# Optimization experiments

Hardware: AMD Instinct MI355X
Metric: run time of the kernel (lower is better)

Reference implementation:

```python
import jax, jax.numpy as jnp
import numpy as np

DEPTH = 3
MAX_NB = 10

def setup_inputs() -> dict:
    key = jax.random.key(0)
    ks = jax.random.split(key, 10)
    B, N, NB, A, E, H = 64, 512, 600, 89, 5, 256
    input_atom = jax.random.normal(ks[0], (B, N, A), dtype=jnp.float32)
    input_bond = jax.random.normal(ks[1], (B, NB, E), dtype=jnp.float32)
    batch_idx = jnp.broadcast_to(jnp.arange(B, dtype=jnp.int32)[:, None, None], (B, N, MAX_NB))
    atom_nei = jax.random.randint(ks[2], (B, N, MAX_NB), 0, N, dtype=jnp.int32)
    bond_nei = jax.random.randint(ks[3], (B, N, MAX_NB), 0, NB, dtype=jnp.int32)
    atom_graph = jnp.stack([batch_idx, atom_nei], axis=-1)  # [B,N,MAX_NB,2]
    bond_graph = jnp.stack([batch_idx, bond_nei], axis=-1)
    num_nbs = jax.random.randint(ks[4], (B, N), 1, MAX_NB + 1, dtype=jnp.int32)
    s = 0.01
    W_atom = s * jax.random.normal(ks[5], (A, H), dtype=jnp.float32)
    W_U2 = s * jax.random.normal(ks[6], (H + E, H), dtype=jnp.float32)
    b_U2 = jnp.zeros((H,), dtype=jnp.float32)
    W_U1 = s * jax.random.normal(ks[7], (2 * H, H), dtype=jnp.float32)
    b_U1 = jnp.zeros((H,), dtype=jnp.float32)
    return {"input_atom": input_atom, "input_bond": input_bond,
            "atom_graph": atom_graph, "bond_graph": bond_graph, "num_nbs": num_nbs,
            "W_atom": W_atom, "W_U2": W_U2, "b_U2": b_U2, "W_U1": W_U1, "b_U1": b_U1}

def reference(input_atom, input_bond, atom_graph, bond_graph, num_nbs,
              W_atom, W_U2, b_U2, W_U1, b_U1):
    # atom embedding: [B,N,H]
    atom_features = input_atom @ W_atom
    # neighbor validity mask [B,N,MAX_NB,1] (tf.sequence_mask)
    mask = (jnp.arange(MAX_NB)[None, None, :] < num_nbs[:, :, None]).astype(atom_features.dtype)[..., None]
    ab, ai = atom_graph[..., 0], atom_graph[..., 1]
    bb, bi = bond_graph[..., 0], bond_graph[..., 1]
    fbond_nei = input_bond[bb, bi]  # [B,N,MAX_NB,5], constant across depth
    for _ in range(DEPTH):
        fatom_nei = atom_features[ab, ai]  # gather_nd -> [B,N,MAX_NB,H]
        l_nei = jnp.concatenate([fatom_nei, fbond_nei], axis=-1)  # [B,N,MAX_NB,H+5]
        pre_label = jax.nn.relu(l_nei @ W_U2 + b_U2)
        nei_label = jnp.sum(pre_label * mask, axis=-2)  # [B,N,H]
        new_label = jnp.concatenate([atom_features, nei_label], axis=-1)  # [B,N,2H]
        atom_features = jax.nn.relu(new_label @ W_U1 + b_U1)
    return atom_features
```

## Files before the change

kernel.cpp:

```cpp
#include <hip/hip_runtime.h>

constexpr int Bb   = 64;
constexpr int Nn   = 512;
constexpr int NBb  = 600;
constexpr int Ad   = 89;
constexpr int Ed   = 5;
constexpr int Hd   = 256;
constexpr int MNB  = 10;
constexpr int Mrows  = Bb * Nn;
constexpr int NBrows = Bb * NBb;
constexpr int Kpad   = 96;

typedef __bf16 bf16x8 __attribute__((ext_vector_type(8)));
typedef float  f32x4  __attribute__((ext_vector_type(4)));

typedef __attribute__((address_space(1))) const void gvoid_t;
typedef __attribute__((address_space(3))) void lvoid_t;

__device__ inline ushort bf_rne(float x) {
  unsigned u = __float_as_uint(x);
  unsigned r = (u + 0x7fffu + ((u >> 16) & 1u)) >> 16;
  return (ushort)r;
}
__device__ inline float bf_f(ushort h) { return __uint_as_float(((unsigned)h) << 16); }

constexpr int S0 = Mrows * Kpad / 256;
constexpr int S1 = NBrows / 8;
constexpr int S2 = Mrows * MNB / 256;
constexpr int S3 = 256;
constexpr int S4 = Kpad * Hd / 256;

__global__ __launch_bounds__(256)
void megaprep(const float* __restrict__ input_atom, const float* __restrict__ input_bond,
              const int* __restrict__ atom_graph, const int* __restrict__ bond_graph,
              const float* __restrict__ W_atom, const float* __restrict__ W_U2,
              const float* __restrict__ b_U2, const float* __restrict__ W_U1,
              ushort* __restrict__ Apadh, ushort* __restrict__ Z, uint* __restrict__ PIdx,
              ushort* __restrict__ w2h, ushort* __restrict__ w1ah, ushort* __restrict__ w1bh,
              ushort* __restrict__ wabf) {
  const int blk = blockIdx.x;
  const int tid = threadIdx.x;
  if (blk < S0) {
    const int e = blk * 256 + tid;
    const int m = e / Kpad, c = e - m * Kpad;
    Apadh[e] = bf_rne(c < Ad ? input_atom[(size_t)m * Ad + c] : 0.f);
  } else if (blk < S0 + S1) {
    const int r0 = (blk - S0) * 8;
    const int h = tid;
    float w[Ed];
#pragma unroll
    for (int e = 0; e < Ed; ++e) w[e] = W_U2[(size_t)(Hd + e) * Hd + h];
    const float b2 = b_U2[h];
#pragma unroll
    for (int j = 0; j < 8; ++j) {
      const int r = r0 + j;
      const float* bp = input_bond + (size_t)r * Ed;
      float d = b2;
#pragma unroll
      for (int e = 0; e < Ed; ++e) d = fmaf(bp[e], w[e], d);
      Z[(size_t)r * Hd + h] = bf_rne(d);
    }
  } else if (blk < S0 + S1 + S2) {
    const int i = (blk - S0 - S1) * 256 + tid;
    const uint ai = (uint)atom_graph[(size_t)i * 2 + 1];
    const uint bi = (uint)bond_graph[(size_t)i * 2 + 1];
    PIdx[i] = (ai << 16) | bi;
  } else if (blk < S0 + S1 + S2 + S3) {
    const int n = blk - S0 - S1 - S2;
    const int k = tid;
    const size_t o = (size_t)n * 256 + k;
    w2h[o]  = bf_rne(W_U2[(size_t)k * Hd + n]);
    w1ah[o] = bf_rne(W_U1[(size_t)k * Hd + n]);
    w1bh[o] = bf_rne(W_U1[(size_t)(k + 256) * Hd + n]);
  } else {
    const int e = (blk - S0 - S1 - S2 - S3) * 256 + tid;
    const int a = e >> 8, h = e & 255;
    wabf[e] = bf_rne((a < Ad) ? W_atom[(size_t)a * Hd + h] : 0.f);
  }
}

__global__ __launch_bounds__(256)
void gemm_wcomb(const ushort* __restrict__ w2h, const ushort* __restrict__ w1ah,
                const ushort* __restrict__ wabf,
                ushort* __restrict__ wc2T, ushort* __restrict__ wc1T) {
  __shared__ ushort As[2][4096];
  __shared__ ushort Bs[2][4096];
  const ushort* Apan = blockIdx.y ? w1ah : w2h;
  ushort*       Cpan = blockIdx.y ? wc1T : wc2T;
  const int tid  = threadIdx.x;
  const int lane = tid & 63;
  const int w    = tid >> 6;
  const int wr   = w >> 1, wc = w & 1;
  const int m0   = blockIdx.x * 128;
  const int arow = tid >> 2;
  const int acol = (tid & 3) * 8;
  const int fr   = lane & 15;
  const int fq   = lane >> 4;

  f32x4 acc[4][4] = {};

  auto stage = [&](int kk, int db) {
#pragma unroll
    for (int i = 0; i < 2; ++i) {
      const ushort* ga = Apan + (size_t)(m0 + arow + 64 * i) * 256 + kk + acol;
      __builtin_amdgcn_global_load_lds((gvoid_t*)ga,
          (lvoid_t*)(&As[db][i * 2048 + w * 512]), 16, 0, 0);
      const int brow = min(arow + 64 * i, Kpad - 1);
      const ushort* gb = wabf + (size_t)brow * 256 + kk + acol;
      __builtin_amdgcn_global_load_lds((gvoid_t*)gb,
          (lvoid_t*)(&Bs[db][i * 2048 + w * 512]), 16, 0, 0);
    }
  };

  stage(0, 0);
  __syncthreads();

#pragma unroll
  for (int ts = 0; ts < 8; ++ts) {
    const int db = ts & 1;
    if (ts + 1 < 8) stage((ts + 1) * 32, db ^ 1);
    bf16x8 bfr[4];
#pragma unroll
    for (int nf = 0; nf < 4; ++nf)
      bfr[nf] = *reinterpret_cast<const bf16x8*>(&Bs[db][(wc * 64 + nf * 16 + fr) * 32 + fq * 8]);
#pragma unroll
    for (int mf = 0; mf < 4; ++mf) {
      bf16x8 af = *reinterpret_cast<const bf16x8*>(&As[db][(wr * 64 + mf * 16 + fr) * 32 + fq * 8]);
#pragma unroll
      for (int nf = 0; nf < 4; ++nf)
        acc[mf][nf] = __builtin_amdgcn_mfma_f32_16x16x32_bf16(af, bfr[nf], acc[mf][nf], 0, 0, 0);
    }
    __syncthreads();
  }

#pragma unroll
  for (int mf = 0; mf < 4; ++mf) {
#pragma unroll
    for (int nf = 0; nf < 4; ++nf) {
      const int col = wc * 64 + nf * 16 + fr;
      if (col < Kpad) {
#pragma unroll
        for (int r = 0; r < 4; ++r) {
          const int row = m0 + wr * 64 + mf * 16 + fq * 4 + r;
          Cpan[(size_t)row * Kpad + col] = bf_rne(acc[mf][nf][r]);
        }
      }
    }
  }
}

template<int KD>
__global__ __launch_bounds__(256)
void gemm_tu(const ushort* __restrict__ A, const ushort* __restrict__ Bt_,
             const ushort* __restrict__ Bp_, const float* __restrict__ bias,
             ushort* __restrict__ Tout, ushort* __restrict__ Pout) {
  constexpr int TS = KD / 32;
  __shared__ ushort As[2][4096];
  __shared__ ushort Bt[2][4096];
  __shared__ ushort Bp[2][4096];
  const int tid  = threadIdx.x;
  const int lane = tid & 63;
  const int w    = tid >> 6;
  const int wr   = w >> 1, wc = w & 1;
  const int m0   = blockIdx.x * 128;
  const int n0   = blockIdx.y * 128;
  const int arow = tid >> 2;
  const int acol = (tid & 3) * 8;
  const int fr   = lane & 15;
  const int fq   = lane >> 4;

  f32x4 accT[4][4] = {};
  f32x4 accP[4][4] = {};

  auto stage = [&](int kk, int db) {
#pragma unroll
    for (int i = 0; i < 2; ++i) {
      const ushort* ga = A + (size_t)(m0 + arow + 64 * i) * KD + kk + acol;
      __builtin_amdgcn_global_load_lds((gvoid_t*)ga,
          (lvoid_t*)(&As[db][i * 2048 + w * 512]), 16, 0, 0);
      const ushort* gt = Bt_ + (size_t)(n0 + arow + 64 * i) * KD + kk + acol;
      __builtin_amdgcn_global_load_lds((gvoid_t*)gt,
          (lvoid_t*)(&Bt[db][i * 2048 + w * 512]), 16, 0, 0);
      const ushort* gp = Bp_ + (size_t)(n0 + arow + 64 * i) * KD + kk + acol;
      __builtin_amdgcn_global_load_lds((gvoid_t*)gp,
          (lvoid_t*)(&Bp[db][i * 2048 + w * 512]), 16, 0, 0);
    }
  };

  stage(0, 0);
  __syncthreads();

#pragma unroll
  for (int ts = 0; ts < TS; ++ts) {
    const int db = ts & 1;
    if (ts + 1 < TS) stage((ts + 1) * 32, db ^ 1);
    bf16x8 bt_[4], bp_[4];
#pragma unroll
    for (int nf = 0; nf < 4; ++nf) {
      bt_[nf] = *reinterpret_cast<const bf16x8*>(&Bt[db][(wc * 64 + nf * 16 + fr) * 32 + fq * 8]);
      bp_[nf] = *reinterpret_cast<const bf16x8*>(&Bp[db][(wc * 64 + nf * 16 + fr) * 32 + fq * 8]);
    }
#pragma unroll
    for (int mf = 0; mf < 4; ++mf) {
      bf16x8 af = *reinterpret_cast<const bf16x8*>(&As[db][(wr * 64 + mf * 16 + fr) * 32 + fq * 8]);
#pragma unroll
      for (int nf = 0; nf < 4; ++nf) {
        accT[mf][nf] = __builtin_amdgcn_mfma_f32_16x16x32_bf16(af, bt_[nf], accT[mf][nf], 0, 0, 0);
        accP[mf][nf] = __builtin_amdgcn_mfma_f32_16x16x32_bf16(af, bp_[nf], accP[mf][nf], 0, 0, 0);
      }
    }
    __syncthreads();
  }

#pragma unroll
  for (int mf = 0; mf < 4; ++mf) {
#pragma unroll
    for (int nf = 0; nf < 4; ++nf) {
      const int col = n0 + wc * 64 + nf * 16 + fr;
      const float bv = bias[col];
#pragma unroll
      for (int r = 0; r < 4; ++r) {
        const int row = m0 + wr * 64 + mf * 16 + fq * 4 + r;
        Tout[(size_t)row * Hd + col] = bf_rne(accT[mf][nf][r]);
        Pout[(size_t)row * Hd + col] = bf_rne(accP[mf][nf][r] + bv);
      }
    }
  }
}

__global__ __launch_bounds__(256)
void gemm_t(const ushort* __restrict__ A, const ushort* __restrict__ B,
            ushort* __restrict__ Chi) {
  __shared__ ushort As[2][4096];
  __shared__ ushort Bs[2][4096];
  const int tid  = threadIdx.x;
  const int lane = tid & 63;
  const int w    = tid >> 6;
  const int wr   = w >> 1, wc = w & 1;
  const int m0   = blockIdx.x * 128;
  const int n0   = blockIdx.y * 128;
  const int arow = tid >> 2;
  const int acol = (tid & 3) * 8;
  const int fr   = lane & 15;
  const int fq   = lane >> 4;

  f32x4 acc[4][4] = {};

  auto stage = [&](int kk, int db) {
#pragma unroll
    for (int i = 0; i < 2; ++i) {
      const ushort* ga = A + (size_t)(m0 + arow + 64 * i) * Hd + kk + acol;
      const ushort* gb = B + (size_t)(n0 + arow + 64 * i) * Hd + kk + acol;
      __builtin_amdgcn_global_load_lds((gvoid_t*)ga,
          (lvoid_t*)(&As[db][i * 2048 + w * 512]), 16, 0, 0);
      __builtin_amdgcn_global_load_lds((gvoid_t*)gb,
          (lvoid_t*)(&Bs[db][i * 2048 + w * 512]), 16, 0, 0);
    }
  };

  stage(0, 0);
  __syncthreads();

#pragma unroll
  for (int ts = 0; ts < 8; ++ts) {
    const int db = ts & 1;
    if (ts + 1 < 8) stage((ts + 1) * 32, db ^ 1);
    bf16x8 bfr[4];
#pragma unroll
    for (int nf = 0; nf < 4; ++nf)
      bfr[nf] = *reinterpret_cast<const bf16x8*>(&Bs[db][(wc * 64 + nf * 16 + fr) * 32 + fq * 8]);
#pragma unroll
    for (int mf = 0; mf < 4; ++mf) {
      bf16x8 af = *reinterpret_cast<const bf16x8*>(&As[db][(wr * 64 + mf * 16 + fr) * 32 + fq * 8]);
#pragma unroll
      for (int nf = 0; nf < 4; ++nf)
        acc[mf][nf] = __builtin_amdgcn_mfma_f32_16x16x32_bf16(af, bfr[nf], acc[mf][nf], 0, 0, 0);
    }
    __syncthreads();
  }

#pragma unroll
  for (int mf = 0; mf < 4; ++mf) {
#pragma unroll
    for (int nf = 0; nf < 4; ++nf) {
      const int col = n0 + wc * 64 + nf * 16 + fr;
#pragma unroll
      for (int r = 0; r < 4; ++r) {
        const int row = m0 + wr * 64 + mf * 16 + fq * 4 + r;
        Chi[(size_t)row * Hd + col] = bf_rne(acc[mf][nf][r]);
      }
    }
  }
}

template<bool FINAL>
__global__ __launch_bounds__(512)
void gemm_k2(const ushort* __restrict__ NEI, const ushort* __restrict__ w1b,
             const ushort* __restrict__ AF, const ushort* __restrict__ w1a,
             const ushort* __restrict__ Pin, const float* __restrict__ bias,
             float* __restrict__ Cf, ushort* __restrict__ Chi) {
  __shared__ ushort As[2][128 * 32];
  __shared__ ushort Bs[2][256 * 32];
  const int tid  = threadIdx.x;
  const int lane = tid & 63;
  const int w    = tid >> 6;
  const int wr   = w >> 1, wc = w & 1;
  const int m0   = blockIdx.x * 128;
  const int fr   = lane & 15;
  const int fq   = lane >> 4;

  f32x4 acc[2][8] = {};

  auto stageA = [&](const ushort* Ap, int kk, int db) {
    const ushort* g = Ap + (size_t)(m0 + (tid >> 2)) * Hd + kk + (tid & 3) * 8;
    __builtin_amdgcn_global_load_lds((gvoid_t*)g,
        (lvoid_t*)(&As[db][w * 512]), 16, 0, 0);
  };
  auto stageB = [&](const ushort* Bp, int kk, int db) {
#pragma unroll
    for (int i = 0; i < 2; ++i) {
      const ushort* g = Bp + (size_t)((tid >> 2) + 128 * i) * Hd + kk + (tid & 3) * 8;
      __builtin_amdgcn_global_load_lds((gvoid_t*)g,
          (lvoid_t*)(&Bs[db][i * 4096 + w * 512]), 16, 0, 0);
    }
  };

  constexpr int TS = FINAL ? 16 : 8;
  if constexpr (FINAL) { stageA(AF, 0, 0); stageB(w1a, 0, 0); }
  else                 { stageA(NEI, 0, 0); stageB(w1b, 0, 0); }
  __syncthreads();

#pragma unroll
  for (int ts = 0; ts < TS; ++ts) {
    const int db = ts & 1;
    if (ts + 1 < TS) {
      const int t2 = ts + 1;
      if constexpr (FINAL) {
        if (t2 < 8) { stageA(AF, t2 * 32, db ^ 1); stageB(w1a, t2 * 32, db ^ 1); }
        else        { stageA(NEI, (t2 - 8) * 32, db ^ 1); stageB(w1b, (t2 - 8) * 32, db ^ 1); }
      } else {
        stageA(NEI, t2 * 32, db ^ 1); stageB(w1b, t2 * 32, db ^ 1);
      }
    }
    bf16x8 bfr[8];
#pragma unroll
    for (int nf = 0; nf < 8; ++nf)
      bfr[nf] = *reinterpret_cast<const bf16x8*>(&Bs[db][(wc * 128 + nf * 16 + fr) * 32 + fq * 8]);
#pragma unroll
    for (int mf = 0; mf < 2; ++mf) {
      bf16x8 af = *reinterpret_cast<const bf16x8*>(&As[db][(wr * 32 + mf * 16 + fr) * 32 + fq * 8]);
#pragma unroll
      for (int nf = 0; nf < 8; ++nf)
        acc[mf][nf] = __builtin_amdgcn_mfma_f32_16x16x32_bf16(af, bfr[nf], acc[mf][nf], 0, 0, 0);
    }
    __syncthreads();
  }

#pragma unroll
  for (int mf = 0; mf < 2; ++mf) {
#pragma unroll
    for (int nf = 0; nf < 8; ++nf) {
      const int col = wc * 128 + nf * 16 + fr;
#pragma unroll
      for (int r = 0; r < 4; ++r) {
        const int row = m0 + wr * 32 + mf * 16 + fq * 4 + r;
        if constexpr (FINAL) {
          Cf[(size_t)row * Hd + col] = fmaxf(acc[mf][nf][r] + bias[col], 0.f);
        } else {
          const float v = fmaxf(acc[mf][nf][r] + bf_f(Pin[(size_t)row * Hd + col]), 0.f);
          Chi[(size_t)row * Hd + col] = bf_rne(v);
        }
      }
    }
  }
}

__global__ __launch_bounds__(256)
void nei_z(const ushort* __restrict__ T, const ushort* __restrict__ Z,
           const uint* __restrict__ PIdx, const int* __restrict__ num_nbs,
           ushort* __restrict__ NEI) {
  const int ho = threadIdx.x & 31;
  const int rp = threadIdx.x >> 5;
  int bid = blockIdx.x;
  bid = (bid & 7) * (gridDim.x >> 3) + (bid >> 3);
  const int m = bid * 8 + rp;
  const int b = m >> 9;
  const int h0 = ho * 8;
  const int nn = num_nbs[m];

  uint pk[MNB];
#pragma unroll
  for (int q = 0; q < 5; ++q) {
    const uint2 u = *reinterpret_cast<const uint2*>(&PIdx[(size_t)m * MNB + q * 2]);
    pk[q * 2] = u.x; pk[q * 2 + 1] = u.y;
  }
  int ai[MNB], bi[MNB];
#pragma unroll
  for (int k = 0; k < MNB; ++k) { ai[k] = (int)(pk[k] >> 16); bi[k] = (int)(pk[k] & 0xffffu); }
#pragma unroll
  for (int k = 1; k < MNB; ++k) {
    ai[k] = (k < nn) ? ai[k] : ai[0];
    bi[k] = (k < nn) ? bi[k] : bi[0];
  }

  float acc[8] = {};
#pragma unroll
  for (int ch = 0; ch < 2; ++ch) {
    uint4 tv[5], zv[5];
#pragma unroll
    for (int k5 = 0; k5 < 5; ++k5) {
      const int k = ch * 5 + k5;
      tv[k5] = *reinterpret_cast<const uint4*>(&T[(((size_t)b << 9) + ai[k]) * Hd + h0]);
      zv[k5] = *reinterpret_cast<const uint4*>(&Z[((size_t)b * NBb + bi[k]) * Hd + h0]);
    }
#pragma unroll
    for (int k5 = 0; k5 < 5; ++k5) {
      const int k = ch * 5 + k5;
      const uint tw[4] = {tv[k5].x, tv[k5].y, tv[k5].z, tv[k5].w};
      const uint zw[4] = {zv[k5].x, zv[k5].y, zv[k5].z, zv[k5].w};
      if (k < nn) {
#pragma unroll
        for (int q = 0; q < 4; ++q) {
          acc[q * 2]     += fmaxf(__uint_as_float(tw[q] << 16) + __uint_as_float(zw[q] << 16), 0.f);
          acc[q * 2 + 1] += fmaxf(__uint_as_float(tw[q] & 0xffff0000u) + __uint_as_float(zw[q] & 0xffff0000u), 0.f);
        }
      }
    }
  }
  uint4 o;
  o.x = (uint)bf_rne(acc[0]) | ((uint)bf_rne(acc[1]) << 16);
  o.y = (uint)bf_rne(acc[2]) | ((uint)bf_rne(acc[3]) << 16);
  o.z = (uint)bf_rne(acc[4]) | ((uint)bf_rne(acc[5]) << 16);
  o.w = (uint)bf_rne(acc[6]) | ((uint)bf_rne(acc[7]) << 16);
  *reinterpret_cast<uint4*>(&NEI[(size_t)m * Hd + h0]) = o;
}

extern "C" void kernel_launch(void* const* d_in, const int* in_sizes, int n_in,
                              void* d_out, int out_size, void* d_ws, size_t ws_size,
                              hipStream_t stream) {
  const float* input_atom = (const float*)d_in[0];
  const float* input_bond = (const float*)d_in[1];
  const int*   atom_graph = (const int*)d_in[2];
  const int*   bond_graph = (const int*)d_in[3];
  const int*   num_nbs    = (const int*)d_in[4];
  const float* W_atom     = (const float*)d_in[5];
  const float* W_U2       = (const float*)d_in[6];
  const float* b_U2       = (const float*)d_in[7];
  const float* W_U1       = (const float*)d_in[8];
  const float* b_U1       = (const float*)d_in[9];

  const size_t SL = (size_t)Mrows * Hd;
  ushort* AFa  = (ushort*)d_ws;
  ushort* AFb  = AFa + SL;
  uint*   PIdx = (uint*)(AFb + SL);
  ushort* w2h  = (ushort*)(PIdx + (size_t)Mrows * MNB);
  ushort* w1ah = w2h  + 256 * 256;
  ushort* w1bh = w1ah + 256 * 256;
  ushort* wabf = w1bh + 256 * 256;
  ushort* wc2T = wabf + Kpad * Hd;
  ushort* wc1T = wc2T + Hd * Kpad;
  ushort* Apadh= wc1T + Hd * Kpad;
  ushort* Zbuf = Apadh + (size_t)Mrows * Kpad;

  ushort* Tbf = (ushort*)d_out;
  ushort* Pbf = Tbf + SL;

  const dim3 blk(256);
  const dim3 gG(Mrows / 128, Hd / 128);
  const dim3 gK(Mrows / 128, 1);

  megaprep<<<S0 + S1 + S2 + S3 + S4, blk, 0, stream>>>(
      input_atom, input_bond, atom_graph, bond_graph, W_atom, W_U2, b_U2, W_U1,
      Apadh, Zbuf, PIdx, w2h, w1ah, w1bh, wabf);

  gemm_wcomb<<<dim3(2, 2), blk, 0, stream>>>(w2h, w1ah, wabf, wc2T, wc1T);

  gemm_tu<Kpad><<<gG, blk, 0, stream>>>(Apadh, wc2T, wc1T, b_U1, Tbf, Pbf);
  nei_z<<<Mrows / 8, blk, 0, stream>>>(Tbf, Zbuf, PIdx, num_nbs, AFb);
  gemm_k2<false><<<gK, 512, 0, stream>>>(AFb, w1bh, nullptr, nullptr, Pbf,
                                         nullptr, nullptr, AFa);

  gemm_tu<Hd><<<gG, blk, 0, stream>>>(AFa, w2h, w1ah, b_U1, Tbf, Pbf);
  nei_z<<<Mrows / 8, blk, 0, stream>>>(Tbf, Zbuf, PIdx, num_nbs, AFb);
  gemm_k2<false><<<gK, 512, 0, stream>>>(AFb, w1bh, nullptr, nullptr, Pbf,
                                         nullptr, nullptr, AFa);

  gemm_t<<<gG, blk, 0, stream>>>(AFa, w2h, Tbf);
  nei_z<<<Mrows / 8, blk, 0, stream>>>(Tbf, Zbuf, PIdx, num_nbs, AFb);
  gemm_k2<true><<<gK, 512, 0, stream>>>(AFb, w1bh, AFa, w1ah, nullptr, b_U1,
                                        (float*)d_out, nullptr);
}
```

Baseline: 160.5 us.

## Fuse neighbor gather-aggregation into the U1 GEMM via an LDS A-tile

The separate nei_z kernel is removed. The masked neighbor gather-sum (relu(T[nei] + Z[bond]) summed over neighbors) is now computed inside the second GEMM kernel and written straight into a swizzled 128x256 bf16 LDS tile, which then serves as the A operand. This avoids writing and re-reading the NEI intermediate in global memory and saves one launch per depth iteration. The cost is that the latency-bound gather now runs on only 256 blocks of 512 threads each, with a large LDS footprint, instead of a wide dedicated grid. That lowers occupancy for the gather and means the gather no longer overlaps with the MFMA stage.

New measurement: 177.9 us. +10.8%, slower.

```diff
diff --git a/kernel.cpp b/kernel.cpp
--- a/kernel.cpp
+++ b/kernel.cpp
@@ -295,12 +295,16 @@
 
 template<bool FINAL>
 __global__ __launch_bounds__(512)
-void gemm_k2(const ushort* __restrict__ NEI, const ushort* __restrict__ w1b,
-             const ushort* __restrict__ AF, const ushort* __restrict__ w1a,
-             const ushort* __restrict__ Pin, const float* __restrict__ bias,
-             float* __restrict__ Cf, ushort* __restrict__ Chi) {
-  __shared__ ushort As[2][128 * 32];
+void gemm_k2g(const ushort* __restrict__ T, const ushort* __restrict__ Z,
+              const uint* __restrict__ PIdx, const int* __restrict__ num_nbs,
+              const ushort* __restrict__ w1b,
+              const ushort* __restrict__ AF, const ushort* __restrict__ w1a,
+              const ushort* __restrict__ Pin, const float* __restrict__ bias,
+              float* __restrict__ Cf, ushort* __restrict__ Chi) {
+  __shared__ ushort Atile[128 * 256];
   __shared__ ushort Bs[2][256 * 32];
+  __shared__ uint   pkL[128 * MNB];
+  __shared__ int    nnL[128];
   const int tid  = threadIdx.x;
   const int lane = tid & 63;
   const int w    = tid >> 6;
@@ -308,14 +312,13 @@
   const int m0   = blockIdx.x * 128;
   const int fr   = lane & 15;
   const int fq   = lane >> 4;
-
-  f32x4 acc[2][8] = {};
-
-  auto stageA = [&](const ushort* Ap, int kk, int db) {
-    const ushort* g = Ap + (size_t)(m0 + (tid >> 2)) * Hd + kk + (tid & 3) * 8;
-    __builtin_amdgcn_global_load_lds((gvoid_t*)g,
-        (lvoid_t*)(&As[db][w * 512]), 16, 0, 0);
-  };
+  const int b    = m0 >> 9;
+  const size_t tb = ((size_t)b << 9) * Hd;
+  const size_t zb = (size_t)b * NBb * Hd;
+
+  for (int i = tid; i < 128 * MNB; i += 512) pkL[i] = PIdx[(size_t)m0 * MNB + i];
+  if (tid < 128) nnL[tid] = num_nbs[m0 + tid];
+
   auto stageB = [&](const ushort* Bp, int kk, int db) {
 #pragma unroll
     for (int i = 0; i < 2; ++i) {
@@ -325,21 +328,71 @@
     }
   };
 
+  stageB(w1b, 0, 0);
+  __syncthreads();
+
+  for (int i = 0; i < 8; ++i) {
+    const int task = tid + i * 512;
+    const int row  = task >> 5;
+    const int ch   = task & 31;
+    const int nn   = nnL[row];
+    const int h0   = ch * 8;
+    float a[8] = {};
+#pragma unroll
+    for (int h5 = 0; h5 < 2; ++h5) {
+      uint4 tv[5], zv[5];
+#pragma unroll
+      for (int j5 = 0; j5 < 5; ++j5) {
+        const int j = h5 * 5 + j5;
+        uint pk = pkL[row * MNB + j];
+        pk = (j < nn) ? pk : pkL[row * MNB];
+        tv[j5] = *reinterpret_cast<const uint4*>(&T[tb + (size_t)(pk >> 16) * Hd + h0]);
+        zv[j5] = *reinterpret_cast<const uint4*>(&Z[zb + (size_t)(pk & 0xffffu) * Hd + h0]);
+      }
+#pragma unroll
+      for (int j5 = 0; j5 < 5; ++j5) {
+        const int j = h5 * 5 + j5;
+        const uint tw[4] = {tv[j5].x, tv[j5].y, tv[j5].z, tv[j5].w};
+        const uint zw[4] = {zv[j5].x, zv[j5].y, zv[j5].z, zv[j5].w};
+        if (j < nn) {
+#pragma unroll
+          for (int q = 0; q < 4; ++q) {
+            a[q * 2]     += fmaxf(__uint_as_float(tw[q] << 16) + __uint_as_float(zw[q] << 16), 0.f);
+            a[q * 2 + 1] += fmaxf(__uint_as_float(tw[q] & 0xffff0000u) + __uint_as_float(zw[q] & 0xffff0000u), 0.f);
+          }
+        }
+      }
+    }
+    uint4 o;
+    o.x = (uint)bf_rne(a[0]) | ((uint)bf_rne(a[1]) << 16);
+    o.y = (uint)bf_rne(a[2]) | ((uint)bf_rne(a[3]) << 16);
+    o.z = (uint)bf_rne(a[4]) | ((uint)bf_rne(a[5]) << 16);
+    o.w = (uint)bf_rne(a[6]) | ((uint)bf_rne(a[7]) << 16);
+    const int byte = row * 512 + ((ch * 16) ^ ((row & 7) << 4));
+    *reinterpret_cast<uint4*>(reinterpret_cast<char*>(Atile) + byte) = o;
+  }
+  __syncthreads();
+
+  f32x4 acc[2][8] = {};
   constexpr int TS = FINAL ? 16 : 8;
-  if constexpr (FINAL) { stageA(AF, 0, 0); stageB(w1a, 0, 0); }
-  else                 { stageA(NEI, 0, 0); stageB(w1b, 0, 0); }
-  __syncthreads();
-
-#pragma unroll
-  for (int ts = 0; ts < TS; ++ts) {
-    const int db = ts & 1;
-    if (ts + 1 < TS) {
-      const int t2 = ts + 1;
+
+  __shared__ ushort Afs[FINAL ? 2 : 1][FINAL ? 128 * 32 : 1];
+  auto stageAF = [&](int kk, int db) {
+    const ushort* g = AF + (size_t)(m0 + (tid >> 2)) * Hd + kk + (tid & 3) * 8;
+    __builtin_amdgcn_global_load_lds((gvoid_t*)g,
+        (lvoid_t*)(&Afs[db][w * 512]), 16, 0, 0);
+  };
+
+#pragma unroll
+  for (int s = 0; s < TS; ++s) {
+    const int db = s & 1;
+    if (s + 1 < TS) {
+      const int t2 = s + 1;
       if constexpr (FINAL) {
-        if (t2 < 8) { stageA(AF, t2 * 32, db ^ 1); stageB(w1a, t2 * 32, db ^ 1); }
-        else        { stageA(NEI, (t2 - 8) * 32, db ^ 1); stageB(w1b, (t2 - 8) * 32, db ^ 1); }
+        if (t2 < 8) stageB(w1b, t2 * 32, db ^ 1);
+        else { stageB(w1a, (t2 - 8) * 32, db ^ 1); stageAF((t2 - 8) * 32, db ^ 1); }
       } else {
-        stageA(NEI, t2 * 32, db ^ 1); stageB(w1b, t2 * 32, db ^ 1);
+        stageB(w1b, t2 * 32, db ^ 1);
       }
     }
     bf16x8 bfr[8];
@@ -348,7 +401,14 @@
       bfr[nf] = *reinterpret_cast<const bf16x8*>(&Bs[db][(wc * 128 + nf * 16 + fr) * 32 + fq * 8]);
 #pragma unroll
     for (int mf = 0; mf < 2; ++mf) {
-      bf16x8 af = *reinterpret_cast<const bf16x8*>(&As[db][(wr * 32 + mf * 16 + fr) * 32 + fq * 8]);
+      const int row = wr * 32 + mf * 16 + fr;
+      bf16x8 af;
+      if (s < 8) {
+        const int byte = row * 512 + (((s & 7) * 64 + fq * 16) ^ ((row & 7) << 4));
+        af = *reinterpret_cast<const bf16x8*>(reinterpret_cast<const char*>(Atile) + byte);
+      } else {
+        af = *reinterpret_cast<const bf16x8*>(&Afs[db][row * 32 + fq * 8]);
+      }
 #pragma unroll
       for (int nf = 0; nf < 8; ++nf)
         acc[mf][nf] = __builtin_amdgcn_mfma_f32_16x16x32_bf16(af, bfr[nf], acc[mf][nf], 0, 0, 0);
@@ -373,66 +433,6 @@
       }
     }
   }
-}
-
-__global__ __launch_bounds__(256)
-void nei_z(const ushort* __restrict__ T, const ushort* __restrict__ Z,
-           const uint* __restrict__ PIdx, const int* __restrict__ num_nbs,
-           ushort* __restrict__ NEI) {
-  const int ho = threadIdx.x & 31;
-  const int rp = threadIdx.x >> 5;
-  int bid = blockIdx.x;
-  bid = (bid & 7) * (gridDim.x >> 3) + (bid >> 3);
-  const int m = bid * 8 + rp;
-  const int b = m >> 9;
-  const int h0 = ho * 8;
-  const int nn = num_nbs[m];
-
-  uint pk[MNB];
-#pragma unroll
-  for (int q = 0; q < 5; ++q) {
-    const uint2 u = *reinterpret_cast<const uint2*>(&PIdx[(size_t)m * MNB + q * 2]);
-    pk[q * 2] = u.x; pk[q * 2 + 1] = u.y;
-  }
-  int ai[MNB], bi[MNB];
-#pragma unroll
-  for (int k = 0; k < MNB; ++k) { ai[k] = (int)(pk[k] >> 16); bi[k] = (int)(pk[k] & 0xffffu); }
-#pragma unroll
-  for (int k = 1; k < MNB; ++k) {
-    ai[k] = (k < nn) ? ai[k] : ai[0];
-    bi[k] = (k < nn) ? bi[k] : bi[0];
-  }
-
-  float acc[8] = {};
-#pragma unroll
-  for (int ch = 0; ch < 2; ++ch) {
-    uint4 tv[5], zv[5];
-#pragma unroll
-    for (int k5 = 0; k5 < 5; ++k5) {
-      const int k = ch * 5 + k5;
-      tv[k5] = *reinterpret_cast<const uint4*>(&T[(((size_t)b << 9) + ai[k]) * Hd + h0]);
-      zv[k5] = *reinterpret_cast<const uint4*>(&Z[((size_t)b * NBb + bi[k]) * Hd + h0]);
-    }
-#pragma unroll
-    for (int k5 = 0; k5 < 5; ++k5) {
-      const int k = ch * 5 + k5;
-      const uint tw[4] = {tv[k5].x, tv[k5].y, tv[k5].z, tv[k5].w};
-      const uint zw[4] = {zv[k5].x, zv[k5].y, zv[k5].z, zv[k5].w};
-      if (k < nn) {
-#pragma unroll
-        for (int q = 0; q < 4; ++q) {
-          acc[q * 2]     += fmaxf(__uint_as_float(tw[q] << 16) + __uint_as_float(zw[q] << 16), 0.f);
-          acc[q * 2 + 1] += fmaxf(__uint_as_float(tw[q] & 0xffff0000u) + __uint_as_float(zw[q] & 0xffff0000u), 0.f);
-        }
-      }
-    }
-  }
-  uint4 o;
-  o.x = (uint)bf_rne(acc[0]) | ((uint)bf_rne(acc[1]) << 16);
-  o.y = (uint)bf_rne(acc[2]) | ((uint)bf_rne(acc[3]) << 16);
-  o.z = (uint)bf_rne(acc[4]) | ((uint)bf_rne(acc[5]) << 16);
-  o.w = (uint)bf_rne(acc[6]) | ((uint)bf_rne(acc[7]) << 16);
-  *reinterpret_cast<uint4*>(&NEI[(size_t)m * Hd + h0]) = o;
 }
 
 extern "C" void kernel_launch(void* const* d_in, const int* in_sizes, int n_in,
@@ -451,8 +451,8 @@
 
   const size_t SL = (size_t)Mrows * Hd;
   ushort* AFa  = (ushort*)d_ws;
-  ushort* AFb  = AFa + SL;
-  uint*   PIdx = (uint*)(AFb + SL);
+  ushort* Tbuf = AFa + SL;
+  uint*   PIdx = (uint*)(Tbuf + SL);
   ushort* w2h  = (ushort*)(PIdx + (size_t)Mrows * MNB);
   ushort* w1ah = w2h  + 256 * 256;
   ushort* w1bh = w1ah + 256 * 256;
@@ -462,8 +462,7 @@
   ushort* Apadh= wc1T + Hd * Kpad;
   ushort* Zbuf = Apadh + (size_t)Mrows * Kpad;
 
-  ushort* Tbf = (ushort*)d_out;
-  ushort* Pbf = Tbf + SL;
+  ushort* Pbf = (ushort*)d_out + SL;
 
   const dim3 blk(256);
   const dim3 gG(Mrows / 128, Hd / 128);
@@ -475,18 +474,18 @@
 
   gemm_wcomb<<<dim3(2, 2), blk, 0, stream>>>(w2h, w1ah, wabf, wc2T, wc1T);
 
-  gemm_tu<Kpad><<<gG, blk, 0, stream>>>(Apadh, wc2T, wc1T, b_U1, Tbf, Pbf);
-  nei_z<<<Mrows / 8, blk, 0, stream>>>(Tbf, Zbuf, PIdx, num_nbs, AFb);
-  gemm_k2<false><<<gK, 512, 0, stream>>>(AFb, w1bh, nullptr, nullptr, Pbf,
-                                         nullptr, nullptr, AFa);
-
-  gemm_tu<Hd><<<gG, blk, 0, stream>>>(AFa, w2h, w1ah, b_U1, Tbf, Pbf);
-  nei_z<<<Mrows / 8, blk, 0, stream>>>(Tbf, Zbuf, PIdx, num_nbs, AFb);
-  gemm_k2<false><<<gK, 512, 0, stream>>>(AFb, w1bh, nullptr, nullptr, Pbf,
-                                         nullptr, nullptr, AFa);
-
-  gemm_t<<<gG, blk, 0, stream>>>(AFa, w2h, Tbf);
-  nei_z<<<Mrows / 8, blk, 0, stream>>>(Tbf, Zbuf, PIdx, num_nbs, AFb);
-  gemm_k2<true><<<gK, 512, 0, stream>>>(AFb, w1bh, AFa, w1ah, nullptr, b_U1,
-                                        (float*)d_out, nullptr);
-}
+  gemm_tu<Kpad><<<gG, blk, 0, stream>>>(Apadh, wc2T, wc1T, b_U1, Tbuf, Pbf);
+  gemm_k2g<false><<<gK, 512, 0, stream>>>(Tbuf, Zbuf, PIdx, num_nbs, w1bh,
+                                          nullptr, nullptr, Pbf, nullptr,
+                                          nullptr, AFa);
+
+  gemm_tu<Hd><<<gG, blk, 0, stream>>>(AFa, w2h, w1ah, b_U1, Tbuf, Pbf);
+  gemm_k2g<false><<<gK, 512, 0, stream>>>(Tbuf, Zbuf, PIdx, num_nbs, w1bh,
+                                          nullptr, nullptr, Pbf, nullptr,
+                                          nullptr, AFa);
+
+  gemm_t<<<gG, blk, 0, stream>>>(AFa, w2h, Tbuf);
+  gemm_k2g<true><<<gK, 512, 0, stream>>>(Tbuf, Zbuf, PIdx, num_nbs, w1bh,
+                                         AFa, w1ah, nullptr, b_U1,
+                                         (float*)d_out, nullptr);
+}
```
